# Kernel optimization log

Hardware: AMD Instinct MI355X
Metric: run time of the kernel (lower is better)

Reference implementation:

```python
import jax, jax.numpy as jnp
import numpy as np
import math

B, S, H, NH = 2, 2048, 2048, 16
HD = H // NH  # 128
NEG = -1e9


def setup_inputs() -> dict:
    key = jax.random.key(0)
    ks = jax.random.split(key, 6)
    x = jax.random.normal(ks[0], (B, S, H), dtype=jnp.float32)
    # realistic rotary frequencies: cos/sin interleaved, shape [S, HD//2, 2]
    inv_freq = 1.0 / (10000.0 ** (np.arange(0, HD, 2, dtype=np.float32) / HD))
    t = np.arange(S, dtype=np.float32)
    ang = np.outer(t, inv_freq)  # [S, HD//2]
    freqs_cis = jnp.asarray(np.stack([np.cos(ang), np.sin(ang)], axis=-1), dtype=jnp.float32)
    # additive causal mask [1,1,S,S]
    causal = jnp.triu(jnp.full((S, S), NEG, dtype=jnp.float32), k=1)[None, None]
    scale = 0.02
    wq = jax.random.normal(ks[1], (H, H), dtype=jnp.float32) * scale
    wk = jax.random.normal(ks[2], (H, H), dtype=jnp.float32) * scale
    wv = jax.random.normal(ks[3], (H, H), dtype=jnp.float32) * scale
    wo = jax.random.normal(ks[4], (H, H), dtype=jnp.float32) * scale
    position_ids = jnp.broadcast_to(jnp.arange(S, dtype=jnp.int64)[None, :], (B, S))
    return {"x": x, "freqs_cis": freqs_cis, "attention_mask": causal,
            "wq": wq, "wk": wk, "wv": wv, "wo": wo, "position_ids": position_ids}


def _apply_rotary(t, freqs):
    # t: [B,S,NH,HD], freqs: [B,S,1,HD//2,2]
    b, s, nh, hd = t.shape
    tp = t.reshape(b, s, nh, hd // 2, 2)
    tr, ti = tp[..., 0], tp[..., 1]
    fr, fi = freqs[..., 0], freqs[..., 1]
    out = jnp.stack([tr * fr - ti * fi, tr * fi + ti * fr], axis=-1)
    return out.reshape(b, s, nh, hd)


def reference(x, freqs_cis, attention_mask, wq, wk, wv, wo, position_ids):
    b, s, h = x.shape
    q = (x @ wq.T).reshape(b, s, NH, HD)
    k = (x @ wk.T).reshape(b, s, NH, HD)
    v = (x @ wv.T).reshape(b, s, NH, HD)
    freqs = freqs_cis[position_ids][:, :, None]  # [B,S,1,HD//2,2]
    q = _apply_rotary(q, freqs)
    k = _apply_rotary(k, freqs)
    # [B,NH,S,HD]
    q = q.transpose(0, 2, 1, 3)
    k = k.transpose(0, 2, 1, 3)
    v = v.transpose(0, 2, 1, 3)
    scores = jnp.einsum('bhqd,bhkd->bhqk', q, k) / math.sqrt(HD)
    scores = scores + attention_mask
    attn = jax.nn.softmax(scores, axis=-1)
    out = jnp.einsum('bhqk,bhkd->bhqd', attn, v)
    out = out.transpose(0, 2, 1, 3).reshape(b, s, h)
    return out @ wo.T
```

## Files before the change

kernel.cpp:

```cpp
#include <hip/hip_runtime.h>

#define DEVI __device__ __forceinline__

typedef unsigned short u16;
typedef unsigned int   u32;
typedef __attribute__((ext_vector_type(4))) float f32x4;
typedef __attribute__((ext_vector_type(8))) short short8;
typedef __attribute__((ext_vector_type(8))) __bf16 bf16x8;

#define B_   2
#define S_   2048
#define H_   2048
#define NH_  16
#define HD_  128
#define BH_  (B_*NH_)
#define QSCALE 0.12751743f

DEVI u16 f2b(float f){
  u32 u = __builtin_bit_cast(u32, f);
  u32 r = (u + 0x7fffu + ((u >> 16) & 1u)) >> 16;
  return (u16)r;
}
DEVI float b2f(u16 h){
  u32 u = ((u32)h) << 16;
  return __builtin_bit_cast(float, u);
}
DEVI u32 cvt_pk_bf16(float lo, float hi){
  u32 r; asm("v_cvt_pk_bf16_f32 %0, %1, %2" : "=v"(r) : "v"(lo), "v"(hi)); return r;
}
DEVI f32x4 mfma_bf16(short8 a, short8 b, f32x4 c){
  return __builtin_amdgcn_mfma_f32_16x16x32_bf16(
      __builtin_bit_cast(bf16x8, a), __builtin_bit_cast(bf16x8, b), c, 0, 0, 0);
}
DEVI void gl_lds16(const void* g, void* l){
  __builtin_amdgcn_global_load_lds((const __attribute__((address_space(1))) void*)g,
                                   (__attribute__((address_space(3))) void*)l, 16, 0, 0);
}

template<int LOG2CPR>
DEVI void stage_swz(const u16* __restrict__ src, int srcStride , u16* lds, int tid){
  const int wid = tid >> 6, lane = tid & 63;
#pragma unroll
  for (int i = 0; i < 4; ++i){
    int lin = i*256 + wid*64 + lane;
    int row = lin >> LOG2CPR;
    int cb  = ((lin & ((1 << LOG2CPR) - 1)) * 16) ^ ((row & 7) << 4);
    gl_lds16(src + (size_t)row * srcStride + (cb >> 1),
             lds + (size_t)(i*256 + wid*64) * 8);
  }
}

__global__ __launch_bounds__(256) void cvt_kernel(const float* __restrict__ src,
                                                  u16* __restrict__ dst, int n4){
  int i = blockIdx.x * 256 + threadIdx.x;
  if (i >= n4) return;
  float4 v = ((const float4*)src)[i];
  u32 lo = (u32)f2b(v.x) | ((u32)f2b(v.y) << 16);
  u32 hi = (u32)f2b(v.z) | ((u32)f2b(v.w) << 16);
  uint2 o; o.x = lo; o.y = hi;
  ((uint2*)dst)[i] = o;
}

template<int EPI>
__global__ __launch_bounds__(256) void gemm_bt(
    const u16* __restrict__ A, const u16* __restrict__ Bw,
    float* __restrict__ C, u16* __restrict__ Qd, u16* __restrict__ Kd, u16* __restrict__ Vd,
    int M, int N, int K)
{
  __shared__ __align__(16) u16 As[128*64];
  __shared__ __align__(16) u16 Bs[128*64];
  const int tid  = threadIdx.x, lane = tid & 63, wid = tid >> 6;
  const int wr   = wid >> 1, wc = wid & 1;
  const int lrow = lane & 15, lk = lane >> 4;
  const int RB = blockIdx.y * 128, CB = blockIdx.x * 128;
  f32x4 acc[4][4] = {};

  for (int k0 = 0; k0 < K; k0 += 64){
    __syncthreads();
    stage_swz<3>(A  + (size_t)RB * K + k0, K, As, tid);
    stage_swz<3>(Bw + (size_t)CB * K + k0, K, Bs, tid);
    __syncthreads();
#pragma unroll
    for (int kk = 0; kk < 2; ++kk){
      short8 af[4], bf[4];
#pragma unroll
      for (int m = 0; m < 4; ++m){
        int row = wr*64 + m*16 + lrow;
        int cb  = (kk*64 + lk*16) ^ ((row & 7) << 4);
        af[m] = *(const short8*)&As[row*64 + (cb >> 1)];
      }
#pragma unroll
      for (int n = 0; n < 4; ++n){
        int row = wc*64 + n*16 + lrow;
        int cb  = (kk*64 + lk*16) ^ ((row & 7) << 4);
        bf[n] = *(const short8*)&Bs[row*64 + (cb >> 1)];
      }
#pragma unroll
      for (int m = 0; m < 4; ++m)
#pragma unroll
        for (int n = 0; n < 4; ++n)
          acc[m][n] = mfma_bf16(af[m], bf[n], acc[m][n]);
    }
  }

#pragma unroll
  for (int m = 0; m < 4; ++m){
#pragma unroll
    for (int n = 0; n < 4; ++n){
#pragma unroll
      for (int r = 0; r < 4; ++r){
        int row = RB + wr*64 + m*16 + lk*4 + r;
        int col = CB + wc*64 + n*16 + lrow;
        float v = acc[m][n][r];
        if constexpr (EPI == 0){
          C[(size_t)row * N + col] = v;
        } else {
          int which = col >> 11;
          int hd = col & 2047;
          int h = hd >> 7, d = hd & 127;
          int b = row >> 11, s = row & 2047;
          u16* dst = (which == 0) ? Qd : (which == 1) ? Kd : Vd;
          dst[(((size_t)(b*NH_ + h)) * S_ + s) * HD_ + d] = f2b(v);
        }
      }
    }
  }
}

__global__ __launch_bounds__(256) void rope_kernel(u16* __restrict__ Q, u16* __restrict__ K,
                                                   const float* __restrict__ F){
  int idx = blockIdx.x * 256 + threadIdx.x;
  int d2 = idx & 63;
  int s  = (idx >> 6) & (S_ - 1);
  int bh = idx >> 17;
  size_t off = ((size_t)bh * S_ + s) * HD_ + d2*2;
  float c = F[s*128 + d2*2], sn = F[s*128 + d2*2 + 1];
  u32 qp = *(const u32*)(Q + off);
  float tr = b2f((u16)qp), ti = b2f((u16)(qp >> 16));
  float q0 = (tr*c - ti*sn) * QSCALE, q1 = (tr*sn + ti*c) * QSCALE;
  *(u32*)(Q + off) = (u32)f2b(q0) | ((u32)f2b(q1) << 16);
  u32 kp = *(const u32*)(K + off);
  tr = b2f((u16)kp); ti = b2f((u16)(kp >> 16));
  float k0 = tr*c - ti*sn, k1 = tr*sn + ti*c;
  *(u32*)(K + off) = (u32)f2b(k0) | ((u32)f2b(k1) << 16);
}

__global__ void transpose_v(const u16* __restrict__ V, u16* __restrict__ Vt){
  __shared__ u16 t[32][33];
  int s0 = blockIdx.x * 32, d0 = blockIdx.y * 32, bh = blockIdx.z;
  const u16* vb = V  + (size_t)bh * S_ * HD_;
  u16*       tb = Vt + (size_t)bh * HD_ * S_;
  int tx = threadIdx.x, ty = threadIdx.y;
#pragma unroll
  for (int i = 0; i < 4; ++i)
    t[ty + i*8][tx] = vb[(size_t)(s0 + ty + i*8) * HD_ + d0 + tx];
  __syncthreads();
#pragma unroll
  for (int i = 0; i < 4; ++i)
    tb[(size_t)(d0 + ty + i*8) * S_ + s0 + tx] = t[tx][ty + i*8];
}

__global__ __launch_bounds__(256) void attn_kernel(
    const u16* __restrict__ Q, const u16* __restrict__ K, const u16* __restrict__ Vt,
    u16* __restrict__ O)
{
  __shared__ __align__(16) u16 Ks[2][64*128];
  __shared__ __align__(16) u16 Vs[2][128*64];
  __shared__ __align__(16) u16 Ps[4][32*64];
  const int tid  = threadIdx.x, lane = tid & 63, wid = tid >> 6;
  const int lrow = lane & 15, lk = lane >> 4;

  const int lin = blockIdx.x;
  const int bh  = (lin & 7) + ((lin >> 6) << 3);
  const int x   = (lin >> 3) & 7;

  const u16* Kb  = K  + (size_t)bh * S_ * HD_;
  const u16* Vtb = Vt + (size_t)bh * HD_ * S_;
  const int b = bh >> 4, h = bh & 15;

  for (int pass = 0; pass < 2; ++pass){
    const int qb = pass ? x : (15 - x);
    const int q0 = qb * 128;
    const int ntile = q0/64 + 2;
    const int qwmax = q0 + wid*32 + 31;

    short8 qf[2][4];
#pragma unroll
    for (int m = 0; m < 2; ++m){
      const u16* qb_ = Q + ((size_t)bh * S_ + q0 + wid*32 + m*16 + lrow) * HD_;
#pragma unroll
      for (int kc = 0; kc < 4; ++kc) qf[m][kc] = *(const short8*)&qb_[kc*32 + lk*8];
    }

    f32x4 acco[2][8] = {};
    float m_[2] = {-3.0e38f, -3.0e38f}, l_[2] = {0.0f, 0.0f};

    int cur = 0;
    stage_swz<4>(Kb,  HD_, &Ks[0][0], tid);
    stage_swz<3>(Vtb, S_,  &Vs[0][0], tid);
    __syncthreads();

    for (int t = 0; t < ntile; ++t){
      if (t + 1 < ntile){
        stage_swz<4>(Kb  + (size_t)(t+1)*64*HD_, HD_, &Ks[cur^1][0], tid);
        stage_swz<3>(Vtb + (t+1)*64,             S_,  &Vs[cur^1][0], tid);
      }
      const int kv0 = t*64;
      if (kv0 <= qwmax){
        const u16* ks = &Ks[cur][0];
        const u16* vs = &Vs[cur][0];

        f32x4 sc[2][4] = {};
        __builtin_amdgcn_s_setprio(1);
#pragma unroll
        for (int nt = 0; nt < 4; ++nt){
          int row = nt*16 + lrow;
#pragma unroll
          for (int kc = 0; kc < 4; ++kc){
            int cb = (kc*64 + lk*16) ^ ((row & 7) << 4);
            short8 kf = *(const short8*)&ks[row*128 + (cb >> 1)];
            sc[0][nt] = mfma_bf16(kf, qf[0][kc], sc[0][nt]);
            sc[1][nt] = mfma_bf16(kf, qf[1][kc], sc[1][nt]);
          }
        }
        __builtin_amdgcn_s_setprio(0);

        if (t >= ntile - 2){
#pragma unroll
          for (int m = 0; m < 2; ++m){
            int qg = q0 + wid*32 + m*16 + lrow;
#pragma unroll
            for (int nt = 0; nt < 4; ++nt)
#pragma unroll
              for (int r = 0; r < 4; ++r)
                if (kv0 + nt*16 + lk*4 + r > qg) sc[m][nt][r] = -1.0e30f;
          }
        }

        u16* pw = &Ps[wid][0];
#pragma unroll
        for (int m = 0; m < 2; ++m){
          float pmax = sc[m][0][0];
#pragma unroll
          for (int nt = 0; nt < 4; ++nt)
#pragma unroll
            for (int r = 0; r < 4; ++r) pmax = fmaxf(pmax, sc[m][nt][r]);
          pmax = fmaxf(pmax, __shfl_xor(pmax, 16));
          pmax = fmaxf(pmax, __shfl_xor(pmax, 32));
          if (!__all(pmax - m_[m] <= 11.0f)){
            float mn = fmaxf(m_[m], pmax);
            float c = exp2f(m_[m] - mn);
            l_[m] *= c;
#pragma unroll
            for (int dt = 0; dt < 8; ++dt)
#pragma unroll
              for (int r = 0; r < 4; ++r) acco[m][dt][r] *= c;
            m_[m] = mn;
          }
          float rs = 0.0f;
#pragma unroll
          for (int nt = 0; nt < 4; ++nt)
#pragma unroll
            for (int r = 0; r < 4; ++r){
              float p = exp2f(sc[m][nt][r] - m_[m]);
              sc[m][nt][r] = p;
              rs += p;
            }
          rs += __shfl_xor(rs, 16);
          rs += __shfl_xor(rs, 32);
          l_[m] += rs;
          int qrow = m*16 + lrow;
#pragma unroll
          for (int nt = 0; nt < 4; ++nt){
            uint2 wv;
            wv.x = cvt_pk_bf16(sc[m][nt][0], sc[m][nt][1]);
            wv.y = cvt_pk_bf16(sc[m][nt][2], sc[m][nt][3]);
            int boff = (nt*32 + lk*8) ^ ((qrow & 7) << 4);
            *(uint2*)((char*)&pw[qrow*64] + boff) = wv;
          }
        }

#pragma unroll
        for (int kc2 = 0; kc2 < 2; ++kc2){
          short8 pf[2];
#pragma unroll
          for (int m = 0; m < 2; ++m){
            int qrow = m*16 + lrow;
            int boff = (kc2*64 + lk*16) ^ ((qrow & 7) << 4);
            pf[m] = *(const short8*)((const char*)&pw[qrow*64] + boff);
          }
          __builtin_amdgcn_s_setprio(1);
#pragma unroll
          for (int dt = 0; dt < 8; ++dt){
            int row = dt*16 + lrow;
            int cb = (kc2*64 + lk*16) ^ ((row & 7) << 4);
            short8 vf = *(const short8*)&vs[row*64 + (cb >> 1)];
            acco[0][dt] = mfma_bf16(vf, pf[0], acco[0][dt]);
            acco[1][dt] = mfma_bf16(vf, pf[1], acco[1][dt]);
          }
          __builtin_amdgcn_s_setprio(0);
        }
      }

      __syncthreads();
      cur ^= 1;
    }

#pragma unroll
    for (int m = 0; m < 2; ++m){
      float inv = 1.0f / l_[m];
      int qg = q0 + wid*32 + m*16 + lrow;
      u16* ob = O + ((size_t)(b*S_ + qg)) * H_ + h*128;
#pragma unroll
      for (int dt = 0; dt < 8; ++dt){
        uint2 wv;
        wv.x = cvt_pk_bf16(acco[m][dt][0]*inv, acco[m][dt][1]*inv);
        wv.y = cvt_pk_bf16(acco[m][dt][2]*inv, acco[m][dt][3]*inv);
        *(uint2*)&ob[dt*16 + lk*4] = wv;
      }
    }
    __syncthreads();
  }
}

extern "C" void kernel_launch(void* const* d_in, const int* in_sizes, int n_in,
                              void* d_out, int out_size, void* d_ws, size_t ws_size,
                              hipStream_t stream)
{
  (void)in_sizes; (void)n_in; (void)out_size; (void)ws_size;
  const float* x  = (const float*)d_in[0];
  const float* fc = (const float*)d_in[1];
  const float* wq = (const float*)d_in[3];
  const float* wk = (const float*)d_in[4];
  const float* wv = (const float*)d_in[5];
  const float* wo = (const float*)d_in[6];

  char* w = (char*)d_ws;
  u16* xb   = (u16*)(w);
  u16* wqkv = (u16*)(w + 16777216);
  u16* wob  = (u16*)(w + 41943040);
  u16* Qr   = (u16*)(w + 50331648);
  u16* Kr   = (u16*)(w + 67108864);
  u16* Vr   = (u16*)(w + 83886080);
  u16* Vt   = (u16*)(w + 100663296);
  u16* aO   = (u16*)(w + 117440512);
  float* out = (float*)d_out;

  cvt_kernel<<<8192, 256, 0, stream>>>(x,  xb,             2097152);
  cvt_kernel<<<4096, 256, 0, stream>>>(wq, wqkv,           1048576);
  cvt_kernel<<<4096, 256, 0, stream>>>(wk, wqkv + 4194304, 1048576);
  cvt_kernel<<<4096, 256, 0, stream>>>(wv, wqkv + 8388608, 1048576);
  cvt_kernel<<<4096, 256, 0, stream>>>(wo, wob,            1048576);

  gemm_bt<1><<<dim3(48, 32), 256, 0, stream>>>(xb, wqkv, nullptr, Qr, Kr, Vr, 4096, 6144, 2048);
  rope_kernel<<<16384, 256, 0, stream>>>(Qr, Kr, fc);
  transpose_v<<<dim3(64, 4, 32), dim3(32, 8), 0, stream>>>(Vr, Vt);
  attn_kernel<<<256, 256, 0, stream>>>(Qr, Kr, Vt, aO);
  gemm_bt<0><<<dim3(16, 32), 256, 0, stream>>>(aO, wob, out, nullptr, nullptr, nullptr, 4096, 2048, 2048);
}
```

Baseline: 294.9 us.

## Fuse RoPE into QKV GEMM epilogue, merge convert launches, precompute staging pointers

Rotary embedding and the Q scaling now run in the QKV GEMM epilogue, using a lane shuffle to fetch the paired element. This removes the separate rope pass, which read and wrote Q and K a second time. The five fp32-to-bf16 conversion launches are merged into one kernel. Global-to-LDS staging addresses in the GEMM and attention loops are computed once and then advanced by a fixed step, so the per-iteration address math goes away. RoPE is now applied in fp32 before bf16 rounding, which slightly changes numerics but should be more accurate.

```diff
diff --git a/kernel.cpp b/kernel.cpp
--- a/kernel.cpp
+++ b/kernel.cpp
@@ -38,34 +38,40 @@
 }
 
 template<int LOG2CPR>
-DEVI void stage_swz(const u16* __restrict__ src, int srcStride , u16* lds, int tid){
-  const int wid = tid >> 6, lane = tid & 63;
+DEVI void stage_ptrs(const u16* src, int srcStride, int tid, const u16* p[4]){
 #pragma unroll
   for (int i = 0; i < 4; ++i){
-    int lin = i*256 + wid*64 + lane;
+    int lin = i*256 + tid;
     int row = lin >> LOG2CPR;
     int cb  = ((lin & ((1 << LOG2CPR) - 1)) * 16) ^ ((row & 7) << 4);
-    gl_lds16(src + (size_t)row * srcStride + (cb >> 1),
-             lds + (size_t)(i*256 + wid*64) * 8);
+    p[i] = src + (size_t)row * srcStride + (cb >> 1);
   }
 }
 
-__global__ __launch_bounds__(256) void cvt_kernel(const float* __restrict__ src,
-                                                  u16* __restrict__ dst, int n4){
+__global__ __launch_bounds__(256) void cvt5_kernel(
+    const float* __restrict__ x,  const float* __restrict__ wq,
+    const float* __restrict__ wk, const float* __restrict__ wv,
+    const float* __restrict__ wo, u16* __restrict__ xb,
+    u16* __restrict__ wqkv, u16* __restrict__ wob){
   int i = blockIdx.x * 256 + threadIdx.x;
-  if (i >= n4) return;
-  float4 v = ((const float4*)src)[i];
-  u32 lo = (u32)f2b(v.x) | ((u32)f2b(v.y) << 16);
-  u32 hi = (u32)f2b(v.z) | ((u32)f2b(v.w) << 16);
-  uint2 o; o.x = lo; o.y = hi;
-  ((uint2*)dst)[i] = o;
+  const float* src; u16* dst; int off;
+  if      (i < 2097152){ src = x;  dst = xb;             off = i;           }
+  else if (i < 3145728){ src = wq; dst = wqkv;           off = i - 2097152; }
+  else if (i < 4194304){ src = wk; dst = wqkv + 4194304; off = i - 3145728; }
+  else if (i < 5242880){ src = wv; dst = wqkv + 8388608; off = i - 4194304; }
+  else                 { src = wo; dst = wob;            off = i - 5242880; }
+  float4 v = ((const float4*)src)[off];
+  uint2 o;
+  o.x = (u32)f2b(v.x) | ((u32)f2b(v.y) << 16);
+  o.y = (u32)f2b(v.z) | ((u32)f2b(v.w) << 16);
+  ((uint2*)dst)[off] = o;
 }
 
 template<int EPI>
 __global__ __launch_bounds__(256) void gemm_bt(
     const u16* __restrict__ A, const u16* __restrict__ Bw,
     float* __restrict__ C, u16* __restrict__ Qd, u16* __restrict__ Kd, u16* __restrict__ Vd,
-    int M, int N, int K)
+    const float* __restrict__ F, int M, int N, int K)
 {
   __shared__ __align__(16) u16 As[128*64];
   __shared__ __align__(16) u16 Bs[128*64];
@@ -75,10 +81,19 @@
   const int RB = blockIdx.y * 128, CB = blockIdx.x * 128;
   f32x4 acc[4][4] = {};
 
+  const u16* asrc[4]; const u16* bsrc[4];
+  stage_ptrs<3>(A  + (size_t)RB * K, K, tid, asrc);
+  stage_ptrs<3>(Bw + (size_t)CB * K, K, tid, bsrc);
+  u16* const adst = &As[(size_t)(tid >> 6) * 512];
+  u16* const bdst = &Bs[(size_t)(tid >> 6) * 512];
+
   for (int k0 = 0; k0 < K; k0 += 64){
     __syncthreads();
-    stage_swz<3>(A  + (size_t)RB * K + k0, K, As, tid);
-    stage_swz<3>(Bw + (size_t)CB * K + k0, K, Bs, tid);
+#pragma unroll
+    for (int i = 0; i < 4; ++i){
+      gl_lds16(asrc[i], adst + i*2048); asrc[i] += 64;
+      gl_lds16(bsrc[i], bdst + i*2048); bsrc[i] += 64;
+    }
     __syncthreads();
 #pragma unroll
     for (int kk = 0; kk < 2; ++kk){
@@ -107,42 +122,30 @@
   for (int m = 0; m < 4; ++m){
 #pragma unroll
     for (int n = 0; n < 4; ++n){
+      const int col = CB + wc*64 + n*16 + lrow;
 #pragma unroll
       for (int r = 0; r < 4; ++r){
-        int row = RB + wr*64 + m*16 + lk*4 + r;
-        int col = CB + wc*64 + n*16 + lrow;
+        const int row = RB + wr*64 + m*16 + lk*4 + r;
         float v = acc[m][n][r];
         if constexpr (EPI == 0){
           C[(size_t)row * N + col] = v;
         } else {
-          int which = col >> 11;
-          int hd = col & 2047;
-          int h = hd >> 7, d = hd & 127;
-          int b = row >> 11, s = row & 2047;
+          const int which = col >> 11;
+          const int hd = col & 2047;
+          const int h = hd >> 7, d = hd & 127;
+          const int b = row >> 11, s = row & 2047;
+          if (which <= 1){
+            float p = __shfl_xor(v, 1);
+            float2 f = *(const float2*)&F[(size_t)s*128 + (d & ~1)];
+            v = (d & 1) ? (v*f.x + p*f.y) : (v*f.x - p*f.y);
+            if (which == 0) v *= QSCALE;
+          }
           u16* dst = (which == 0) ? Qd : (which == 1) ? Kd : Vd;
           dst[(((size_t)(b*NH_ + h)) * S_ + s) * HD_ + d] = f2b(v);
         }
       }
     }
   }
-}
-
-__global__ __launch_bounds__(256) void rope_kernel(u16* __restrict__ Q, u16* __restrict__ K,
-                                                   const float* __restrict__ F){
-  int idx = blockIdx.x * 256 + threadIdx.x;
-  int d2 = idx & 63;
-  int s  = (idx >> 6) & (S_ - 1);
-  int bh = idx >> 17;
-  size_t off = ((size_t)bh * S_ + s) * HD_ + d2*2;
-  float c = F[s*128 + d2*2], sn = F[s*128 + d2*2 + 1];
-  u32 qp = *(const u32*)(Q + off);
-  float tr = b2f((u16)qp), ti = b2f((u16)(qp >> 16));
-  float q0 = (tr*c - ti*sn) * QSCALE, q1 = (tr*sn + ti*c) * QSCALE;
-  *(u32*)(Q + off) = (u32)f2b(q0) | ((u32)f2b(q1) << 16);
-  u32 kp = *(const u32*)(K + off);
-  tr = b2f((u16)kp); ti = b2f((u16)(kp >> 16));
-  float k0 = tr*c - ti*sn, k1 = tr*sn + ti*c;
-  *(u32*)(K + off) = (u32)f2b(k0) | ((u32)f2b(k1) << 16);
 }
 
 __global__ void transpose_v(const u16* __restrict__ V, u16* __restrict__ Vt){
@@ -178,6 +181,10 @@
   const u16* Vtb = Vt + (size_t)bh * HD_ * S_;
   const int b = bh >> 4, h = bh & 15;
 
+  u16* const kld = &Ks[0][(size_t)wid * 512];
+  u16* const vld = &Vs[0][(size_t)wid * 512];
+  const int bufstep = 64*128;
+
   for (int pass = 0; pass < 2; ++pass){
     const int qb = pass ? x : (15 - x);
     const int q0 = qb * 128;
@@ -192,18 +199,29 @@
       for (int kc = 0; kc < 4; ++kc) qf[m][kc] = *(const short8*)&qb_[kc*32 + lk*8];
     }
 
+    const u16* kp[4]; const u16* vp[4];
+    stage_ptrs<4>(Kb,  HD_, tid, kp);
+    stage_ptrs<3>(Vtb, S_,  tid, vp);
+
     f32x4 acco[2][8] = {};
     float m_[2] = {-3.0e38f, -3.0e38f}, l_[2] = {0.0f, 0.0f};
 
     int cur = 0;
-    stage_swz<4>(Kb,  HD_, &Ks[0][0], tid);
-    stage_swz<3>(Vtb, S_,  &Vs[0][0], tid);
+#pragma unroll
+    for (int i = 0; i < 4; ++i){
+      gl_lds16(kp[i], kld + i*2048); kp[i] += 64*HD_;
+      gl_lds16(vp[i], vld + i*2048); vp[i] += 64;
+    }
     __syncthreads();
 
     for (int t = 0; t < ntile; ++t){
       if (t + 1 < ntile){
-        stage_swz<4>(Kb  + (size_t)(t+1)*64*HD_, HD_, &Ks[cur^1][0], tid);
-        stage_swz<3>(Vtb + (t+1)*64,             S_,  &Vs[cur^1][0], tid);
+        const int bo = (cur^1) * bufstep;
+#pragma unroll
+        for (int i = 0; i < 4; ++i){
+          gl_lds16(kp[i], kld + bo + i*2048); kp[i] += 64*HD_;
+          gl_lds16(vp[i], vld + bo + i*2048); vp[i] += 64;
+        }
       }
       const int kv0 = t*64;
       if (kv0 <= qwmax){
@@ -346,15 +364,10 @@
   u16* aO   = (u16*)(w + 117440512);
   float* out = (float*)d_out;
 
-  cvt_kernel<<<8192, 256, 0, stream>>>(x,  xb,             2097152);
-  cvt_kernel<<<4096, 256, 0, stream>>>(wq, wqkv,           1048576);
-  cvt_kernel<<<4096, 256, 0, stream>>>(wk, wqkv + 4194304, 1048576);
-  cvt_kernel<<<4096, 256, 0, stream>>>(wv, wqkv + 8388608, 1048576);
-  cvt_kernel<<<4096, 256, 0, stream>>>(wo, wob,            1048576);
-
-  gemm_bt<1><<<dim3(48, 32), 256, 0, stream>>>(xb, wqkv, nullptr, Qr, Kr, Vr, 4096, 6144, 2048);
-  rope_kernel<<<16384, 256, 0, stream>>>(Qr, Kr, fc);
+  cvt5_kernel<<<24576, 256, 0, stream>>>(x, wq, wk, wv, wo, xb, wqkv, wob);
+
+  gemm_bt<1><<<dim3(48, 32), 256, 0, stream>>>(xb, wqkv, nullptr, Qr, Kr, Vr, fc, 4096, 6144, 2048);
   transpose_v<<<dim3(64, 4, 32), dim3(32, 8), 0, stream>>>(Vr, Vt);
   attn_kernel<<<256, 256, 0, stream>>>(Qr, Kr, Vt, aO);
-  gemm_bt<0><<<dim3(16, 32), 256, 0, stream>>>(aO, wob, out, nullptr, nullptr, nullptr, 4096, 2048, 2048);
-}
+  gemm_bt<0><<<dim3(16, 32), 256, 0, stream>>>(aO, wob, out, nullptr, nullptr, nullptr, nullptr, 4096, 2048, 2048);
+}
```

New measurement: 319.6 us. 8.4% more time.

## Read K/V fragments directly from global in attention and merge conversion launches

Applied to the files above, without the earlier changes.

The attention kernel drops its shared-memory double-buffered K/V staging and block-wide barriers. Each wave now loads K and transposed-V MFMA fragments straight from global memory, relying on L1/L2 cache reuse, and runs only the tiles its own causal range needs. The five fp32-to-bf16 conversion launches are merged into one kernel. This removes LDS traffic, syncs and launch overhead, but exposes global load latency without prefetching and makes the four waves of a block fetch the same K/V data repeatedly.

```diff
diff --git a/kernel.cpp b/kernel.cpp
--- a/kernel.cpp
+++ b/kernel.cpp
@@ -50,15 +50,23 @@
   }
 }
 
-__global__ __launch_bounds__(256) void cvt_kernel(const float* __restrict__ src,
-                                                  u16* __restrict__ dst, int n4){
+__global__ __launch_bounds__(256) void cvt5_kernel(
+    const float* __restrict__ x,  const float* __restrict__ wq,
+    const float* __restrict__ wk, const float* __restrict__ wv,
+    const float* __restrict__ wo, u16* __restrict__ xb,
+    u16* __restrict__ wqkv, u16* __restrict__ wob){
   int i = blockIdx.x * 256 + threadIdx.x;
-  if (i >= n4) return;
-  float4 v = ((const float4*)src)[i];
-  u32 lo = (u32)f2b(v.x) | ((u32)f2b(v.y) << 16);
-  u32 hi = (u32)f2b(v.z) | ((u32)f2b(v.w) << 16);
-  uint2 o; o.x = lo; o.y = hi;
-  ((uint2*)dst)[i] = o;
+  const float* src; u16* dst; int off;
+  if      (i < 2097152){ src = x;  dst = xb;             off = i;           }
+  else if (i < 3145728){ src = wq; dst = wqkv;           off = i - 2097152; }
+  else if (i < 4194304){ src = wk; dst = wqkv + 4194304; off = i - 3145728; }
+  else if (i < 5242880){ src = wv; dst = wqkv + 8388608; off = i - 4194304; }
+  else                 { src = wo; dst = wob;            off = i - 5242880; }
+  float4 v = ((const float4*)src)[off];
+  uint2 o;
+  o.x = (u32)f2b(v.x) | ((u32)f2b(v.y) << 16);
+  o.y = (u32)f2b(v.z) | ((u32)f2b(v.w) << 16);
+  ((uint2*)dst)[off] = o;
 }
 
 template<int EPI>
@@ -164,8 +172,6 @@
     const u16* __restrict__ Q, const u16* __restrict__ K, const u16* __restrict__ Vt,
     u16* __restrict__ O)
 {
-  __shared__ __align__(16) u16 Ks[2][64*128];
-  __shared__ __align__(16) u16 Vs[2][128*64];
   __shared__ __align__(16) u16 Ps[4][32*64];
   const int tid  = threadIdx.x, lane = tid & 63, wid = tid >> 6;
   const int lrow = lane & 15, lk = lane >> 4;
@@ -178,132 +184,114 @@
   const u16* Vtb = Vt + (size_t)bh * HD_ * S_;
   const int b = bh >> 4, h = bh & 15;
 
+  const u16* kbase = Kb  + (size_t)lrow * HD_ + lk*8;
+  const u16* vbase = Vtb + (size_t)lrow * S_  + lk*8;
+  u16* const pw = &Ps[wid][0];
+
   for (int pass = 0; pass < 2; ++pass){
     const int qb = pass ? x : (15 - x);
     const int q0 = qb * 128;
-    const int ntile = q0/64 + 2;
-    const int qwmax = q0 + wid*32 + 31;
+    const int ntw = ((q0 + wid*32 + 31) >> 6) + 1;
 
     short8 qf[2][4];
 #pragma unroll
     for (int m = 0; m < 2; ++m){
-      const u16* qb_ = Q + ((size_t)bh * S_ + q0 + wid*32 + m*16 + lrow) * HD_;
-#pragma unroll
-      for (int kc = 0; kc < 4; ++kc) qf[m][kc] = *(const short8*)&qb_[kc*32 + lk*8];
+      const u16* qp_ = Q + ((size_t)bh * S_ + q0 + wid*32 + m*16 + lrow) * HD_;
+#pragma unroll
+      for (int kc = 0; kc < 4; ++kc) qf[m][kc] = *(const short8*)&qp_[kc*32 + lk*8];
     }
 
     f32x4 acco[2][8] = {};
     float m_[2] = {-3.0e38f, -3.0e38f}, l_[2] = {0.0f, 0.0f};
 
-    int cur = 0;
-    stage_swz<4>(Kb,  HD_, &Ks[0][0], tid);
-    stage_swz<3>(Vtb, S_,  &Vs[0][0], tid);
-    __syncthreads();
-
-    for (int t = 0; t < ntile; ++t){
-      if (t + 1 < ntile){
-        stage_swz<4>(Kb  + (size_t)(t+1)*64*HD_, HD_, &Ks[cur^1][0], tid);
-        stage_swz<3>(Vtb + (t+1)*64,             S_,  &Vs[cur^1][0], tid);
-      }
+    for (int t = 0; t < ntw; ++t){
       const int kv0 = t*64;
-      if (kv0 <= qwmax){
-        const u16* ks = &Ks[cur][0];
-        const u16* vs = &Vs[cur][0];
-
-        f32x4 sc[2][4] = {};
-        __builtin_amdgcn_s_setprio(1);
+
+      f32x4 sc[2][4] = {};
+      const u16* kt = kbase + (size_t)kv0 * HD_;
+      __builtin_amdgcn_s_setprio(1);
+#pragma unroll
+      for (int nt = 0; nt < 4; ++nt){
+#pragma unroll
+        for (int kc = 0; kc < 4; ++kc){
+          short8 kf = *(const short8*)&kt[(size_t)nt*16*HD_ + kc*32];
+          sc[0][nt] = mfma_bf16(kf, qf[0][kc], sc[0][nt]);
+          sc[1][nt] = mfma_bf16(kf, qf[1][kc], sc[1][nt]);
+        }
+      }
+      __builtin_amdgcn_s_setprio(0);
+
+      if (kv0 >= q0){
+#pragma unroll
+        for (int m = 0; m < 2; ++m){
+          int qg = q0 + wid*32 + m*16 + lrow;
+#pragma unroll
+          for (int nt = 0; nt < 4; ++nt)
+#pragma unroll
+            for (int r = 0; r < 4; ++r)
+              if (kv0 + nt*16 + lk*4 + r > qg) sc[m][nt][r] = -1.0e30f;
+        }
+      }
+
+#pragma unroll
+      for (int m = 0; m < 2; ++m){
+        float pmax = sc[m][0][0];
+#pragma unroll
+        for (int nt = 0; nt < 4; ++nt)
+#pragma unroll
+          for (int r = 0; r < 4; ++r) pmax = fmaxf(pmax, sc[m][nt][r]);
+        pmax = fmaxf(pmax, __shfl_xor(pmax, 16));
+        pmax = fmaxf(pmax, __shfl_xor(pmax, 32));
+        if (!__all(pmax - m_[m] <= 11.0f)){
+          float mn = fmaxf(m_[m], pmax);
+          float c = exp2f(m_[m] - mn);
+          l_[m] *= c;
+#pragma unroll
+          for (int dt = 0; dt < 8; ++dt)
+#pragma unroll
+            for (int r = 0; r < 4; ++r) acco[m][dt][r] *= c;
+          m_[m] = mn;
+        }
+        float rs = 0.0f;
+#pragma unroll
+        for (int nt = 0; nt < 4; ++nt)
+#pragma unroll
+          for (int r = 0; r < 4; ++r){
+            float p = exp2f(sc[m][nt][r] - m_[m]);
+            sc[m][nt][r] = p;
+            rs += p;
+          }
+        rs += __shfl_xor(rs, 16);
+        rs += __shfl_xor(rs, 32);
+        l_[m] += rs;
+        int qrow = m*16 + lrow;
 #pragma unroll
         for (int nt = 0; nt < 4; ++nt){
-          int row = nt*16 + lrow;
-#pragma unroll
-          for (int kc = 0; kc < 4; ++kc){
-            int cb = (kc*64 + lk*16) ^ ((row & 7) << 4);
-            short8 kf = *(const short8*)&ks[row*128 + (cb >> 1)];
-            sc[0][nt] = mfma_bf16(kf, qf[0][kc], sc[0][nt]);
-            sc[1][nt] = mfma_bf16(kf, qf[1][kc], sc[1][nt]);
-          }
-        }
-        __builtin_amdgcn_s_setprio(0);
-
-        if (t >= ntile - 2){
-#pragma unroll
-          for (int m = 0; m < 2; ++m){
-            int qg = q0 + wid*32 + m*16 + lrow;
-#pragma unroll
-            for (int nt = 0; nt < 4; ++nt)
-#pragma unroll
-              for (int r = 0; r < 4; ++r)
-                if (kv0 + nt*16 + lk*4 + r > qg) sc[m][nt][r] = -1.0e30f;
-          }
-        }
-
-        u16* pw = &Ps[wid][0];
+          uint2 wv;
+          wv.x = cvt_pk_bf16(sc[m][nt][0], sc[m][nt][1]);
+          wv.y = cvt_pk_bf16(sc[m][nt][2], sc[m][nt][3]);
+          int boff = (nt*32 + lk*8) ^ ((qrow & 7) << 4);
+          *(uint2*)((char*)&pw[qrow*64] + boff) = wv;
+        }
+      }
+
+      const u16* vt0 = vbase + kv0;
+#pragma unroll
+      for (int kc2 = 0; kc2 < 2; ++kc2){
+        short8 pf[2];
 #pragma unroll
         for (int m = 0; m < 2; ++m){
-          float pmax = sc[m][0][0];
-#pragma unroll
-          for (int nt = 0; nt < 4; ++nt)
-#pragma unroll
-            for (int r = 0; r < 4; ++r) pmax = fmaxf(pmax, sc[m][nt][r]);
-          pmax = fmaxf(pmax, __shfl_xor(pmax, 16));
-          pmax = fmaxf(pmax, __shfl_xor(pmax, 32));
-          if (!__all(pmax - m_[m] <= 11.0f)){
-            float mn = fmaxf(m_[m], pmax);
-            float c = exp2f(m_[m] - mn);
-            l_[m] *= c;
-#pragma unroll
-            for (int dt = 0; dt < 8; ++dt)
-#pragma unroll
-              for (int r = 0; r < 4; ++r) acco[m][dt][r] *= c;
-            m_[m] = mn;
-          }
-          float rs = 0.0f;
-#pragma unroll
-          for (int nt = 0; nt < 4; ++nt)
-#pragma unroll
-            for (int r = 0; r < 4; ++r){
-              float p = exp2f(sc[m][nt][r] - m_[m]);
-              sc[m][nt][r] = p;
-              rs += p;
-            }
-          rs += __shfl_xor(rs, 16);
-          rs += __shfl_xor(rs, 32);
-          l_[m] += rs;
           int qrow = m*16 + lrow;
-#pragma unroll
-          for (int nt = 0; nt < 4; ++nt){
-            uint2 wv;
-            wv.x = cvt_pk_bf16(sc[m][nt][0], sc[m][nt][1]);
-            wv.y = cvt_pk_bf16(sc[m][nt][2], sc[m][nt][3]);
-            int boff = (nt*32 + lk*8) ^ ((qrow & 7) << 4);
-            *(uint2*)((char*)&pw[qrow*64] + boff) = wv;
-          }
-        }
-
-#pragma unroll
-        for (int kc2 = 0; kc2 < 2; ++kc2){
-          short8 pf[2];
-#pragma unroll
-          for (int m = 0; m < 2; ++m){
-            int qrow = m*16 + lrow;
-            int boff = (kc2*64 + lk*16) ^ ((qrow & 7) << 4);
-            pf[m] = *(const short8*)((const char*)&pw[qrow*64] + boff);
-          }
-          __builtin_amdgcn_s_setprio(1);
-#pragma unroll
-          for (int dt = 0; dt < 8; ++dt){
-            int row = dt*16 + lrow;
-            int cb = (kc2*64 + lk*16) ^ ((row & 7) << 4);
-            short8 vf = *(const short8*)&vs[row*64 + (cb >> 1)];
-            acco[0][dt] = mfma_bf16(vf, pf[0], acco[0][dt]);
-            acco[1][dt] = mfma_bf16(vf, pf[1], acco[1][dt]);
-          }
-          __builtin_amdgcn_s_setprio(0);
-        }
-      }
-
-      __syncthreads();
-      cur ^= 1;
+          int boff = (kc2*64 + lk*16) ^ ((qrow & 7) << 4);
+          pf[m] = *(const short8*)((const char*)&pw[qrow*64] + boff);
+        }
+#pragma unroll
+        for (int dt = 0; dt < 8; ++dt){
+          short8 vf = *(const short8*)&vt0[(size_t)dt*16*S_ + kc2*32];
+          acco[0][dt] = mfma_bf16(vf, pf[0], acco[0][dt]);
+          acco[1][dt] = mfma_bf16(vf, pf[1], acco[1][dt]);
+        }
+      }
     }
 
 #pragma unroll
@@ -319,7 +307,6 @@
         *(uint2*)&ob[dt*16 + lk*4] = wv;
       }
     }
-    __syncthreads();
   }
 }
 
@@ -346,11 +333,7 @@
   u16* aO   = (u16*)(w + 117440512);
   float* out = (float*)d_out;
 
-  cvt_kernel<<<8192, 256, 0, stream>>>(x,  xb,             2097152);
-  cvt_kernel<<<4096, 256, 0, stream>>>(wq, wqkv,           1048576);
-  cvt_kernel<<<4096, 256, 0, stream>>>(wk, wqkv + 4194304, 1048576);
-  cvt_kernel<<<4096, 256, 0, stream>>>(wv, wqkv + 8388608, 1048576);
-  cvt_kernel<<<4096, 256, 0, stream>>>(wo, wob,            1048576);
+  cvt5_kernel<<<24576, 256, 0, stream>>>(x, wq, wk, wv, wo, xb, wqkv, wob);
 
   gemm_bt<1><<<dim3(48, 32), 256, 0, stream>>>(xb, wqkv, nullptr, Qr, Kr, Vr, 4096, 6144, 2048);
   rope_kernel<<<16384, 256, 0, stream>>>(Qr, Kr, fc);
```

Result: slower. 382.4 us (+29.7%).

## Split attention into one block per query tile, fuse Q rope, merge casts

Applied to the files above, without the earlier changes.

The attention kernel now launches 512 blocks, each handling a single 128-row query tile, instead of 256 blocks that each looped over a paired heavy and light tile. Blocks are ordered so the long causal tiles are scheduled first. The rotary embedding and the softmax scale for Q are applied in registers while Q fragments are loaded inside attention, so the separate rope pass now only touches K. The five fp32-to-bf16 conversion launches are merged into one kernel that picks its source by index range. The aim is better CU occupancy and load balance in attention, less Q read/write traffic, and fewer launches. The cost is that per-block load balance now depends on the hardware scheduler rather than explicit pairing.

```diff
diff --git a/kernel.cpp b/kernel.cpp
--- a/kernel.cpp
+++ b/kernel.cpp
@@ -28,6 +28,10 @@
 DEVI u32 cvt_pk_bf16(float lo, float hi){
   u32 r; asm("v_cvt_pk_bf16_f32 %0, %1, %2" : "=v"(r) : "v"(lo), "v"(hi)); return r;
 }
+DEVI u32 rot2(u16 lo, u16 hi, float c, float s, float scale){
+  float tr = b2f(lo), ti = b2f(hi);
+  return cvt_pk_bf16((tr*c - ti*s)*scale, (tr*s + ti*c)*scale);
+}
 DEVI f32x4 mfma_bf16(short8 a, short8 b, f32x4 c){
   return __builtin_amdgcn_mfma_f32_16x16x32_bf16(
       __builtin_bit_cast(bf16x8, a), __builtin_bit_cast(bf16x8, b), c, 0, 0, 0);
@@ -50,15 +54,23 @@
   }
 }
 
-__global__ __launch_bounds__(256) void cvt_kernel(const float* __restrict__ src,
-                                                  u16* __restrict__ dst, int n4){
+__global__ __launch_bounds__(256) void cvt5_kernel(
+    const float* __restrict__ x,  const float* __restrict__ wq,
+    const float* __restrict__ wk, const float* __restrict__ wv,
+    const float* __restrict__ wo, u16* __restrict__ xb,
+    u16* __restrict__ wqkv, u16* __restrict__ wob){
   int i = blockIdx.x * 256 + threadIdx.x;
-  if (i >= n4) return;
-  float4 v = ((const float4*)src)[i];
-  u32 lo = (u32)f2b(v.x) | ((u32)f2b(v.y) << 16);
-  u32 hi = (u32)f2b(v.z) | ((u32)f2b(v.w) << 16);
-  uint2 o; o.x = lo; o.y = hi;
-  ((uint2*)dst)[i] = o;
+  const float* src; u16* dst; int off;
+  if      (i < 2097152){ src = x;  dst = xb;             off = i;           }
+  else if (i < 3145728){ src = wq; dst = wqkv;           off = i - 2097152; }
+  else if (i < 4194304){ src = wk; dst = wqkv + 4194304; off = i - 3145728; }
+  else if (i < 5242880){ src = wv; dst = wqkv + 8388608; off = i - 4194304; }
+  else                 { src = wo; dst = wob;            off = i - 5242880; }
+  float4 v = ((const float4*)src)[off];
+  uint2 o;
+  o.x = (u32)f2b(v.x) | ((u32)f2b(v.y) << 16);
+  o.y = (u32)f2b(v.z) | ((u32)f2b(v.w) << 16);
+  ((uint2*)dst)[off] = o;
 }
 
 template<int EPI>
@@ -127,22 +139,17 @@
   }
 }
 
-__global__ __launch_bounds__(256) void rope_kernel(u16* __restrict__ Q, u16* __restrict__ K,
-                                                   const float* __restrict__ F){
+__global__ __launch_bounds__(256) void rope_k_kernel(u16* __restrict__ K,
+                                                     const float* __restrict__ F){
   int idx = blockIdx.x * 256 + threadIdx.x;
   int d2 = idx & 63;
   int s  = (idx >> 6) & (S_ - 1);
   int bh = idx >> 17;
   size_t off = ((size_t)bh * S_ + s) * HD_ + d2*2;
   float c = F[s*128 + d2*2], sn = F[s*128 + d2*2 + 1];
-  u32 qp = *(const u32*)(Q + off);
-  float tr = b2f((u16)qp), ti = b2f((u16)(qp >> 16));
-  float q0 = (tr*c - ti*sn) * QSCALE, q1 = (tr*sn + ti*c) * QSCALE;
-  *(u32*)(Q + off) = (u32)f2b(q0) | ((u32)f2b(q1) << 16);
   u32 kp = *(const u32*)(K + off);
-  tr = b2f((u16)kp); ti = b2f((u16)(kp >> 16));
-  float k0 = tr*c - ti*sn, k1 = tr*sn + ti*c;
-  *(u32*)(K + off) = (u32)f2b(k0) | ((u32)f2b(k1) << 16);
+  float tr = b2f((u16)kp), ti = b2f((u16)(kp >> 16));
+  *(u32*)(K + off) = (u32)f2b(tr*c - ti*sn) | ((u32)f2b(tr*sn + ti*c) << 16);
 }
 
 __global__ void transpose_v(const u16* __restrict__ V, u16* __restrict__ Vt){
@@ -162,7 +169,7 @@
 
 __global__ __launch_bounds__(256) void attn_kernel(
     const u16* __restrict__ Q, const u16* __restrict__ K, const u16* __restrict__ Vt,
-    u16* __restrict__ O)
+    const float* __restrict__ F, u16* __restrict__ O)
 {
   __shared__ __align__(16) u16 Ks[2][64*128];
   __shared__ __align__(16) u16 Vs[2][128*64];
@@ -171,155 +178,163 @@
   const int lrow = lane & 15, lk = lane >> 4;
 
   const int lin = blockIdx.x;
-  const int bh  = (lin & 7) + ((lin >> 6) << 3);
-  const int x   = (lin >> 3) & 7;
+  const int bh   = (lin & 7) | (((lin >> 3) & 3) << 3);
+  const int sidx = (lin >> 5) & 7;
+  const int qb   = (lin < 256) ? (15 - sidx) : sidx;
+  const int q0 = qb * 128;
+  const int ntile = 2*qb + 2;
+  const int qwmax = q0 + wid*32 + 31;
 
   const u16* Kb  = K  + (size_t)bh * S_ * HD_;
   const u16* Vtb = Vt + (size_t)bh * HD_ * S_;
   const int b = bh >> 4, h = bh & 15;
-
-  for (int pass = 0; pass < 2; ++pass){
-    const int qb = pass ? x : (15 - x);
-    const int q0 = qb * 128;
-    const int ntile = q0/64 + 2;
-    const int qwmax = q0 + wid*32 + 31;
-
-    short8 qf[2][4];
-#pragma unroll
-    for (int m = 0; m < 2; ++m){
-      const u16* qb_ = Q + ((size_t)bh * S_ + q0 + wid*32 + m*16 + lrow) * HD_;
-#pragma unroll
-      for (int kc = 0; kc < 4; ++kc) qf[m][kc] = *(const short8*)&qb_[kc*32 + lk*8];
-    }
-
-    f32x4 acco[2][8] = {};
-    float m_[2] = {-3.0e38f, -3.0e38f}, l_[2] = {0.0f, 0.0f};
-
-    int cur = 0;
-    stage_swz<4>(Kb,  HD_, &Ks[0][0], tid);
-    stage_swz<3>(Vtb, S_,  &Vs[0][0], tid);
+  u16* const pw = &Ps[wid][0];
+
+  short8 qf[2][4];
+#pragma unroll
+  for (int m = 0; m < 2; ++m){
+    const int qg = q0 + wid*32 + m*16 + lrow;
+    const u16* qp_ = Q + ((size_t)bh * S_ + qg) * HD_;
+    const float* Fq = F + (size_t)qg * 128;
+#pragma unroll
+    for (int kc = 0; kc < 4; ++kc){
+      short8 q = *(const short8*)&qp_[kc*32 + lk*8];
+      float4 fa = *(const float4*)&Fq[kc*32 + lk*8];
+      float4 fb = *(const float4*)&Fq[kc*32 + lk*8 + 4];
+      uint4 w;
+      w.x = rot2((u16)q[0], (u16)q[1], fa.x, fa.y, QSCALE);
+      w.y = rot2((u16)q[2], (u16)q[3], fa.z, fa.w, QSCALE);
+      w.z = rot2((u16)q[4], (u16)q[5], fb.x, fb.y, QSCALE);
+      w.w = rot2((u16)q[6], (u16)q[7], fb.z, fb.w, QSCALE);
+      qf[m][kc] = __builtin_bit_cast(short8, w);
+    }
+  }
+
+  f32x4 acco[2][8] = {};
+  float m_[2] = {-3.0e38f, -3.0e38f}, l_[2] = {0.0f, 0.0f};
+
+  int cur = 0;
+  stage_swz<4>(Kb,  HD_, &Ks[0][0], tid);
+  stage_swz<3>(Vtb, S_,  &Vs[0][0], tid);
+  __syncthreads();
+
+  for (int t = 0; t < ntile; ++t){
+    if (t + 1 < ntile){
+      stage_swz<4>(Kb  + (size_t)(t+1)*64*HD_, HD_, &Ks[cur^1][0], tid);
+      stage_swz<3>(Vtb + (t+1)*64,             S_,  &Vs[cur^1][0], tid);
+    }
+    const int kv0 = t*64;
+    if (kv0 <= qwmax){
+      const u16* ks = &Ks[cur][0];
+      const u16* vs = &Vs[cur][0];
+
+      f32x4 sc[2][4] = {};
+      __builtin_amdgcn_s_setprio(1);
+#pragma unroll
+      for (int nt = 0; nt < 4; ++nt){
+        int row = nt*16 + lrow;
+#pragma unroll
+        for (int kc = 0; kc < 4; ++kc){
+          int cb = (kc*64 + lk*16) ^ ((row & 7) << 4);
+          short8 kf = *(const short8*)&ks[row*128 + (cb >> 1)];
+          sc[0][nt] = mfma_bf16(kf, qf[0][kc], sc[0][nt]);
+          sc[1][nt] = mfma_bf16(kf, qf[1][kc], sc[1][nt]);
+        }
+      }
+      __builtin_amdgcn_s_setprio(0);
+
+      if (t >= ntile - 2){
+#pragma unroll
+        for (int m = 0; m < 2; ++m){
+          int qg = q0 + wid*32 + m*16 + lrow;
+#pragma unroll
+          for (int nt = 0; nt < 4; ++nt)
+#pragma unroll
+            for (int r = 0; r < 4; ++r)
+              if (kv0 + nt*16 + lk*4 + r > qg) sc[m][nt][r] = -1.0e30f;
+        }
+      }
+
+#pragma unroll
+      for (int m = 0; m < 2; ++m){
+        float pmax = sc[m][0][0];
+#pragma unroll
+        for (int nt = 0; nt < 4; ++nt)
+#pragma unroll
+          for (int r = 0; r < 4; ++r) pmax = fmaxf(pmax, sc[m][nt][r]);
+        pmax = fmaxf(pmax, __shfl_xor(pmax, 16));
+        pmax = fmaxf(pmax, __shfl_xor(pmax, 32));
+        if (!__all(pmax - m_[m] <= 11.0f)){
+          float mn = fmaxf(m_[m], pmax);
+          float c = exp2f(m_[m] - mn);
+          l_[m] *= c;
+#pragma unroll
+          for (int dt = 0; dt < 8; ++dt)
+#pragma unroll
+            for (int r = 0; r < 4; ++r) acco[m][dt][r] *= c;
+          m_[m] = mn;
+        }
+        float rs = 0.0f;
+#pragma unroll
+        for (int nt = 0; nt < 4; ++nt)
+#pragma unroll
+          for (int r = 0; r < 4; ++r){
+            float p = exp2f(sc[m][nt][r] - m_[m]);
+            sc[m][nt][r] = p;
+            rs += p;
+          }
+        rs += __shfl_xor(rs, 16);
+        rs += __shfl_xor(rs, 32);
+        l_[m] += rs;
+        int qrow = m*16 + lrow;
+#pragma unroll
+        for (int nt = 0; nt < 4; ++nt){
+          uint2 wv;
+          wv.x = cvt_pk_bf16(sc[m][nt][0], sc[m][nt][1]);
+          wv.y = cvt_pk_bf16(sc[m][nt][2], sc[m][nt][3]);
+          int boff = (nt*32 + lk*8) ^ ((qrow & 7) << 4);
+          *(uint2*)((char*)&pw[qrow*64] + boff) = wv;
+        }
+      }
+
+#pragma unroll
+      for (int kc2 = 0; kc2 < 2; ++kc2){
+        short8 pf[2];
+#pragma unroll
+        for (int m = 0; m < 2; ++m){
+          int qrow = m*16 + lrow;
+          int boff = (kc2*64 + lk*16) ^ ((qrow & 7) << 4);
+          pf[m] = *(const short8*)((const char*)&pw[qrow*64] + boff);
+        }
+        __builtin_amdgcn_s_setprio(1);
+#pragma unroll
+        for (int dt = 0; dt < 8; ++dt){
+          int row = dt*16 + lrow;
+          int cb = (kc2*64 + lk*16) ^ ((row & 7) << 4);
+          short8 vf = *(const short8*)&vs[row*64 + (cb >> 1)];
+          acco[0][dt] = mfma_bf16(vf, pf[0], acco[0][dt]);
+          acco[1][dt] = mfma_bf16(vf, pf[1], acco[1][dt]);
+        }
+        __builtin_amdgcn_s_setprio(0);
+      }
+    }
+
     __syncthreads();
-
-    for (int t = 0; t < ntile; ++t){
-      if (t + 1 < ntile){
-        stage_swz<4>(Kb  + (size_t)(t+1)*64*HD_, HD_, &Ks[cur^1][0], tid);
-        stage_swz<3>(Vtb + (t+1)*64,             S_,  &Vs[cur^1][0], tid);
-      }
-      const int kv0 = t*64;
-      if (kv0 <= qwmax){
-        const u16* ks = &Ks[cur][0];
-        const u16* vs = &Vs[cur][0];
-
-        f32x4 sc[2][4] = {};
-        __builtin_amdgcn_s_setprio(1);
-#pragma unroll
-        for (int nt = 0; nt < 4; ++nt){
-          int row = nt*16 + lrow;
-#pragma unroll
-          for (int kc = 0; kc < 4; ++kc){
-            int cb = (kc*64 + lk*16) ^ ((row & 7) << 4);
-            short8 kf = *(const short8*)&ks[row*128 + (cb >> 1)];
-            sc[0][nt] = mfma_bf16(kf, qf[0][kc], sc[0][nt]);
-            sc[1][nt] = mfma_bf16(kf, qf[1][kc], sc[1][nt]);
-          }
-        }
-        __builtin_amdgcn_s_setprio(0);
-
-        if (t >= ntile - 2){
-#pragma unroll
-          for (int m = 0; m < 2; ++m){
-            int qg = q0 + wid*32 + m*16 + lrow;
-#pragma unroll
-            for (int nt = 0; nt < 4; ++nt)
-#pragma unroll
-              for (int r = 0; r < 4; ++r)
-                if (kv0 + nt*16 + lk*4 + r > qg) sc[m][nt][r] = -1.0e30f;
-          }
-        }
-
-        u16* pw = &Ps[wid][0];
-#pragma unroll
-        for (int m = 0; m < 2; ++m){
-          float pmax = sc[m][0][0];
-#pragma unroll
-          for (int nt = 0; nt < 4; ++nt)
-#pragma unroll
-            for (int r = 0; r < 4; ++r) pmax = fmaxf(pmax, sc[m][nt][r]);
-          pmax = fmaxf(pmax, __shfl_xor(pmax, 16));
-          pmax = fmaxf(pmax, __shfl_xor(pmax, 32));
-          if (!__all(pmax - m_[m] <= 11.0f)){
-            float mn = fmaxf(m_[m], pmax);
-            float c = exp2f(m_[m] - mn);
-            l_[m] *= c;
-#pragma unroll
-            for (int dt = 0; dt < 8; ++dt)
-#pragma unroll
-              for (int r = 0; r < 4; ++r) acco[m][dt][r] *= c;
-            m_[m] = mn;
-          }
-          float rs = 0.0f;
-#pragma unroll
-          for (int nt = 0; nt < 4; ++nt)
-#pragma unroll
-            for (int r = 0; r < 4; ++r){
-              float p = exp2f(sc[m][nt][r] - m_[m]);
-              sc[m][nt][r] = p;
-              rs += p;
-            }
-          rs += __shfl_xor(rs, 16);
-          rs += __shfl_xor(rs, 32);
-          l_[m] += rs;
-          int qrow = m*16 + lrow;
-#pragma unroll
-          for (int nt = 0; nt < 4; ++nt){
-            uint2 wv;
-            wv.x = cvt_pk_bf16(sc[m][nt][0], sc[m][nt][1]);
-            wv.y = cvt_pk_bf16(sc[m][nt][2], sc[m][nt][3]);
-            int boff = (nt*32 + lk*8) ^ ((qrow & 7) << 4);
-            *(uint2*)((char*)&pw[qrow*64] + boff) = wv;
-          }
-        }
-
-#pragma unroll
-        for (int kc2 = 0; kc2 < 2; ++kc2){
-          short8 pf[2];
-#pragma unroll
-          for (int m = 0; m < 2; ++m){
-            int qrow = m*16 + lrow;
-            int boff = (kc2*64 + lk*16) ^ ((qrow & 7) << 4);
-            pf[m] = *(const short8*)((const char*)&pw[qrow*64] + boff);
-          }
-          __builtin_amdgcn_s_setprio(1);
-#pragma unroll
-          for (int dt = 0; dt < 8; ++dt){
-            int row = dt*16 + lrow;
-            int cb = (kc2*64 + lk*16) ^ ((row & 7) << 4);
-            short8 vf = *(const short8*)&vs[row*64 + (cb >> 1)];
-            acco[0][dt] = mfma_bf16(vf, pf[0], acco[0][dt]);
-            acco[1][dt] = mfma_bf16(vf, pf[1], acco[1][dt]);
-          }
-          __builtin_amdgcn_s_setprio(0);
-        }
-      }
-
-      __syncthreads();
-      cur ^= 1;
-    }
-
-#pragma unroll
-    for (int m = 0; m < 2; ++m){
-      float inv = 1.0f / l_[m];
-      int qg = q0 + wid*32 + m*16 + lrow;
-      u16* ob = O + ((size_t)(b*S_ + qg)) * H_ + h*128;
-#pragma unroll
-      for (int dt = 0; dt < 8; ++dt){
-        uint2 wv;
-        wv.x = cvt_pk_bf16(acco[m][dt][0]*inv, acco[m][dt][1]*inv);
-        wv.y = cvt_pk_bf16(acco[m][dt][2]*inv, acco[m][dt][3]*inv);
-        *(uint2*)&ob[dt*16 + lk*4] = wv;
-      }
-    }
-    __syncthreads();
+    cur ^= 1;
+  }
+
+#pragma unroll
+  for (int m = 0; m < 2; ++m){
+    float inv = 1.0f / l_[m];
+    int qg = q0 + wid*32 + m*16 + lrow;
+    u16* ob = O + ((size_t)(b*S_ + qg)) * H_ + h*128;
+#pragma unroll
+    for (int dt = 0; dt < 8; ++dt){
+      uint2 wv;
+      wv.x = cvt_pk_bf16(acco[m][dt][0]*inv, acco[m][dt][1]*inv);
+      wv.y = cvt_pk_bf16(acco[m][dt][2]*inv, acco[m][dt][3]*inv);
+      *(uint2*)&ob[dt*16 + lk*4] = wv;
+    }
   }
 }
 
@@ -346,15 +361,11 @@
   u16* aO   = (u16*)(w + 117440512);
   float* out = (float*)d_out;
 
-  cvt_kernel<<<8192, 256, 0, stream>>>(x,  xb,             2097152);
-  cvt_kernel<<<4096, 256, 0, stream>>>(wq, wqkv,           1048576);
-  cvt_kernel<<<4096, 256, 0, stream>>>(wk, wqkv + 4194304, 1048576);
-  cvt_kernel<<<4096, 256, 0, stream>>>(wv, wqkv + 8388608, 1048576);
-  cvt_kernel<<<4096, 256, 0, stream>>>(wo, wob,            1048576);
+  cvt5_kernel<<<24576, 256, 0, stream>>>(x, wq, wk, wv, wo, xb, wqkv, wob);
 
   gemm_bt<1><<<dim3(48, 32), 256, 0, stream>>>(xb, wqkv, nullptr, Qr, Kr, Vr, 4096, 6144, 2048);
-  rope_kernel<<<16384, 256, 0, stream>>>(Qr, Kr, fc);
+  rope_k_kernel<<<16384, 256, 0, stream>>>(Kr, fc);
   transpose_v<<<dim3(64, 4, 32), dim3(32, 8), 0, stream>>>(Vr, Vt);
-  attn_kernel<<<256, 256, 0, stream>>>(Qr, Kr, Vt, aO);
+  attn_kernel<<<512, 256, 0, stream>>>(Qr, Kr, Vt, fc, aO);
   gemm_bt<0><<<dim3(16, 32), 256, 0, stream>>>(aO, wob, out, nullptr, nullptr, nullptr, 4096, 2048, 2048);
 }
```

Result: slower. 309.7 us (+5.0%).
